# Kernel optimization log

Hardware: AMD Instinct MI355X
Metric: run time of the kernel (lower is better)

The kernel has to match this reference:

```python
import jax, jax.numpy as jnp
import numpy as np

N = 100_000   # nodes
E = 3_200_000 # edges
D = 128       # input feature dim


def setup_inputs() -> dict:
    key = jax.random.key(0)
    ks = jax.random.split(key, 6)
    x = jax.random.normal(ks[0], (N, D), dtype=jnp.float32)
    edge_index = jax.random.randint(ks[1], (2, E), 0, N, dtype=jnp.int32)
    # Glorot-ish init for the three GCN layer weights
    W1 = jax.random.normal(ks[2], (D, 32), dtype=jnp.float32) * (1.0 / np.sqrt(D))
    W2 = jax.random.normal(ks[3], (32, 16), dtype=jnp.float32) * (1.0 / np.sqrt(32))
    W3 = jax.random.normal(ks[4], (16, 1), dtype=jnp.float32) * (1.0 / np.sqrt(16))
    b1 = jnp.zeros((32,), jnp.float32)
    b2 = jnp.zeros((16,), jnp.float32)
    b3 = jnp.zeros((1,), jnp.float32)
    return {"x": x, "edge_index": edge_index, "W1": W1, "b1": b1,
            "W2": W2, "b2": b2, "W3": W3, "b3": b3}


def _gcn_edges(edge_index, num_nodes):
    # PyG GCNConv default: add self-loops, symmetric normalization
    loop = jnp.arange(num_nodes, dtype=edge_index.dtype)
    src = jnp.concatenate([edge_index[0], loop])
    dst = jnp.concatenate([edge_index[1], loop])
    deg = jax.ops.segment_sum(jnp.ones_like(dst, jnp.float32), dst, num_segments=num_nodes)
    dis = jax.lax.rsqrt(deg)  # deg >= 1 because of self-loops
    norm = dis[src] * dis[dst]  # [E+N]
    return src, dst, norm


def _gcn_layer(h, W, b, src, dst, norm, num_nodes):
    # linear transform, then normalized gather -> scatter-add aggregation
    hw = h @ W                                  # [N, out]
    msg = norm[:, None] * hw[src]               # [E+N, out]
    out = jax.ops.segment_sum(msg, dst, num_segments=num_nodes)
    return out + b


def reference(x, edge_index, W1, b1, W2, b2, W3, b3):
    src, dst, norm = _gcn_edges(edge_index, N)
    h = jax.nn.relu(_gcn_layer(x, W1, b1, src, dst, norm, N))
    h = jax.nn.relu(_gcn_layer(h, W2, b2, src, dst, norm, N))
    return _gcn_layer(h, W3, b3, src, dst, norm, N)  # [N, 1]
```

## Files before the change

kernel.cpp:

```cpp
#include <hip/hip_runtime.h>
#include <hip/hip_fp16.h>

#define NN 100000
#define NE 3200000
#define DI 128

#define RSH 8
#define RMASK 255
#define NB ((NN + RMASK) >> RSH)
#define CAP 9472
#define SB 256
#define SCHUNK ((NE + SB - 1) / SB)
#define MAXE ((SCHUNK + 1023) / 1024)
#define SK ((CAP + 1023) / 1024)

#define OFF_GCUR   ((size_t)100000)
#define OFF_ROWPTR ((size_t)100800)
#define OFF_DEG    ((size_t)200800)
#define OFF_REC    ((size_t)300800)
#define OFF_HWD1   (OFF_REC + (size_t)NB * CAP)
#define OFF_HWD2   (OFF_HWD1 + (size_t)16 * NN)
#define OFF_HWD3   (OFF_HWD2 + (size_t)8 * NN)

#define ACC8(r) { const __half2* hp_ = reinterpret_cast<const __half2*>(&(r));      \
    float2 f0_ = __half22float2(hp_[0]), f1_ = __half22float2(hp_[1]);              \
    float2 f2_ = __half22float2(hp_[2]), f3_ = __half22float2(hp_[3]);              \
    a0 += f0_.x; a1 += f0_.y; a2 += f1_.x; a3 += f1_.y;                             \
    a4 += f2_.x; a5 += f2_.y; a6 += f3_.x; a7 += f3_.y; }

__global__ __launch_bounds__(1024) void scatter_kernel(const int* __restrict__ src,
                                                       const int* __restrict__ dst,
                                                       int* __restrict__ gcur,
                                                       unsigned* __restrict__ rec) {
    __shared__ unsigned lrec[SCHUNK];
    __shared__ unsigned short lbkt[SCHUNK];
    __shared__ int lh[NB];
    __shared__ int lofs[NB];
    __shared__ int lbase[NB];
    int tid = threadIdx.x;
    for (int i = tid; i < NB; i += 1024) lh[i] = 0;
    __syncthreads();
    int base = blockIdx.x * SCHUNK;
    int end = min(base + SCHUNK, NE);
    int cnt_total = end - base;
    int keys[MAXE], rank[MAXE];
#pragma unroll
    for (int i = 0; i < MAXE; i++) {
        int e = base + tid + i * 1024;
        bool ok = e < end;
        keys[i] = ok ? dst[e] : 0;
        rank[i] = ok ? atomicAdd(&lh[keys[i] >> RSH], 1) : 0;
    }
    __syncthreads();
    int* stmp = (int*)lrec;
    int v = (tid < NB) ? lh[tid] : 0;
    stmp[tid] = v;
    __syncthreads();
    for (int d = 1; d < 1024; d <<= 1) {
        int t = (tid >= d) ? stmp[tid - d] : 0;
        __syncthreads();
        stmp[tid] += t;
        __syncthreads();
    }
    if (tid < NB) {
        lofs[tid] = stmp[tid] - v;
        lbase[tid] = v ? atomicAdd(&gcur[tid], v) : 0;
    }
    __syncthreads();
#pragma unroll
    for (int i = 0; i < MAXE; i++) {
        int e = base + tid + i * 1024;
        if (e < end) {
            int d = keys[i];
            int b = d >> RSH;
            int slot = lofs[b] + rank[i];
            lrec[slot] = ((unsigned)src[e] << RSH) | (unsigned)(d & RMASK);
            lbkt[slot] = (unsigned short)b;
        }
    }
    __syncthreads();
    for (int j = tid; j < cnt_total; j += 1024) {
        int b = lbkt[j];
        int pos = lbase[b] + (j - lofs[b]);
        if (pos < CAP)
            rec[(size_t)b * CAP + pos] = lrec[j];
    }
}

__global__ __launch_bounds__(1024) void sort_kernel(const int* __restrict__ gcur,
                                                    unsigned* __restrict__ rec,
                                                    int* __restrict__ rowptr,
                                                    int* __restrict__ deg,
                                                    float* __restrict__ dis) {
    __shared__ int cnt[256];
    __shared__ int sc[256];
    int tid = threadIdx.x, b = blockIdx.x;
    if (tid < 256) cnt[tid] = 0;
    __syncthreads();
    int count = min(gcur[b], CAP);
    size_t rbeg = (size_t)b * CAP;
    unsigned myrec[SK];
    int myrank[SK];
#pragma unroll
    for (int k = 0; k < SK; k++) {
        int j = tid + k * 1024;
        if (j < count) {
            unsigned r = rec[rbeg + j];
            myrec[k] = r;
            myrank[k] = atomicAdd(&cnt[r & RMASK], 1);
        } else {
            myrec[k] = 0; myrank[k] = 0;
        }
    }
    __syncthreads();
    if (tid < 256) sc[tid] = cnt[tid];
    __syncthreads();
    for (int d = 1; d < 256; d <<= 1) {
        int v = (tid < 256 && tid >= d) ? sc[tid - d] : 0;
        __syncthreads();
        if (tid < 256) sc[tid] += v;
        __syncthreads();
    }
    if (tid < 256) {
        int excl = sc[tid] - cnt[tid];
        int node = (b << RSH) + tid;
        if (node < NN) {
            rowptr[node] = (int)rbeg + excl;
            deg[node] = cnt[tid];
            dis[node] = rsqrtf((float)cnt[tid] + 1.0f);
        }
        cnt[tid] = excl;
    }
    __syncthreads();
#pragma unroll
    for (int k = 0; k < SK; k++) {
        int j = tid + k * 1024;
        if (j < count) {
            unsigned r = myrec[k];
            int pos = cnt[r & RMASK] + myrank[k];
            rec[rbeg + pos] = r >> RSH;
        }
    }
}

__global__ __launch_bounds__(256) void gemm1_kernel(const float* __restrict__ x,
                                                    const float* __restrict__ W,
                                                    const float* __restrict__ dis,
                                                    __half* __restrict__ out) {
    __shared__ float Ws[DI][32];
    __shared__ float xs[32][DI + 4];
    int tid = threadIdx.x;
    for (int i4 = tid; i4 < DI * 32 / 4; i4 += 256) {
        float4 w = reinterpret_cast<const float4*>(W)[i4];
        int base = i4 * 4;
        *reinterpret_cast<float4*>(&Ws[base / 32][base % 32]) = w;
    }
    int node0 = blockIdx.x * 32;
    for (int i4 = tid; i4 < 32 * DI / 4; i4 += 256) {
        int base = i4 * 4;
        int nl = base / DI, k = base % DI;
        int node = node0 + nl;
        float4 v = (node < NN) ? reinterpret_cast<const float4*>(x)[((size_t)node * DI + k) / 4]
                               : make_float4(0.f, 0.f, 0.f, 0.f);
        *reinterpret_cast<float4*>(&xs[nl][k]) = v;
    }
    __syncthreads();
    int nl = tid >> 3;
    int c4 = (tid & 7) * 4;
    int node = node0 + nl;
    if (node >= NN) return;
    float a0 = 0.f, a1 = 0.f, a2 = 0.f, a3 = 0.f;
#pragma unroll 8
    for (int k4 = 0; k4 < DI; k4 += 4) {
        float4 xv = *reinterpret_cast<const float4*>(&xs[nl][k4]);
        float4 w0 = *reinterpret_cast<const float4*>(&Ws[k4 + 0][c4]);
        float4 w1 = *reinterpret_cast<const float4*>(&Ws[k4 + 1][c4]);
        float4 w2 = *reinterpret_cast<const float4*>(&Ws[k4 + 2][c4]);
        float4 w3 = *reinterpret_cast<const float4*>(&Ws[k4 + 3][c4]);
        a0 += xv.x * w0.x + xv.y * w1.x + xv.z * w2.x + xv.w * w3.x;
        a1 += xv.x * w0.y + xv.y * w1.y + xv.z * w2.y + xv.w * w3.y;
        a2 += xv.x * w0.z + xv.y * w1.z + xv.z * w2.z + xv.w * w3.z;
        a3 += xv.x * w0.w + xv.y * w1.w + xv.z * w2.w + xv.w * w3.w;
    }
    float dn = dis[node];
    __half2 h0 = __floats2half2_rn(dn * a0, dn * a1);
    __half2 h1 = __floats2half2_rn(dn * a2, dn * a3);
    __half2* op = reinterpret_cast<__half2*>(out + (size_t)node * 32 + c4);
    op[0] = h0;
    op[1] = h1;
}

__global__ __launch_bounds__(256) void agg32_fused_kernel(const int* __restrict__ rowptr,
                                                          const int* __restrict__ deg,
                                                          const int* __restrict__ srcs,
                                                          const __half* __restrict__ hwd1,
                                                          const float* __restrict__ dis,
                                                          const float* __restrict__ b1,
                                                          const float* __restrict__ W2,
                                                          __half2* __restrict__ hwd2) {
    __shared__ float hc[64][33];
    __shared__ float W2s[32][16];
    int tid = threadIdx.x;
    for (int i = tid; i < 512; i += 256) W2s[i >> 4][i & 15] = W2[i];
    int gtid = blockIdx.x * 256 + tid;
    int node = gtid >> 2;
    int lane = tid & 3;
    int nl = tid >> 2;
    int c8 = lane * 8;
    if (node < NN) {
        int beg = rowptr[node];
        int end = beg + deg[node];
        const float4* hv = reinterpret_cast<const float4*>(hwd1);
        float a0, a1, a2, a3, a4, a5, a6, a7;
        {
            float4 sr = hv[(size_t)node * 4 + lane];
            const __half2* hp = reinterpret_cast<const __half2*>(&sr);
            float2 f0 = __half22float2(hp[0]), f1 = __half22float2(hp[1]);
            float2 f2 = __half22float2(hp[2]), f3 = __half22float2(hp[3]);
            a0 = f0.x; a1 = f0.y; a2 = f1.x; a3 = f1.y;
            a4 = f2.x; a5 = f2.y; a6 = f3.x; a7 = f3.y;
        }
        int j = beg;
        for (; j + 8 <= end; j += 8) {
            int i0 = srcs[j],     i1 = srcs[j + 1], i2 = srcs[j + 2], i3 = srcs[j + 3];
            int i4 = srcs[j + 4], i5 = srcs[j + 5], i6 = srcs[j + 6], i7 = srcs[j + 7];
            float4 r0 = hv[(size_t)i0 * 4 + lane];
            float4 r1 = hv[(size_t)i1 * 4 + lane];
            float4 r2 = hv[(size_t)i2 * 4 + lane];
            float4 r3 = hv[(size_t)i3 * 4 + lane];
            float4 r4 = hv[(size_t)i4 * 4 + lane];
            float4 r5 = hv[(size_t)i5 * 4 + lane];
            float4 r6 = hv[(size_t)i6 * 4 + lane];
            float4 r7 = hv[(size_t)i7 * 4 + lane];
            ACC8(r0); ACC8(r1); ACC8(r2); ACC8(r3);
            ACC8(r4); ACC8(r5); ACC8(r6); ACC8(r7);
        }
        for (; j < end; j++) {
            float4 r = hv[(size_t)srcs[j] * 4 + lane];
            ACC8(r);
        }
        float dn = dis[node];
        hc[nl][c8 + 0] = fmaxf(dn * a0 + b1[c8 + 0], 0.f);
        hc[nl][c8 + 1] = fmaxf(dn * a1 + b1[c8 + 1], 0.f);
        hc[nl][c8 + 2] = fmaxf(dn * a2 + b1[c8 + 2], 0.f);
        hc[nl][c8 + 3] = fmaxf(dn * a3 + b1[c8 + 3], 0.f);
        hc[nl][c8 + 4] = fmaxf(dn * a4 + b1[c8 + 4], 0.f);
        hc[nl][c8 + 5] = fmaxf(dn * a5 + b1[c8 + 5], 0.f);
        hc[nl][c8 + 6] = fmaxf(dn * a6 + b1[c8 + 6], 0.f);
        hc[nl][c8 + 7] = fmaxf(dn * a7 + b1[c8 + 7], 0.f);
    }
    __syncthreads();
    int node0 = blockIdx.x * 64;
    for (int o = tid; o < 64 * 8; o += 256) {
        int l = o >> 3, cp = o & 7;
        int n2 = node0 + l;
        if (n2 < NN) {
            float s0 = 0.f, s1 = 0.f;
#pragma unroll
            for (int k = 0; k < 32; k++) {
                float h = hc[l][k];
                s0 += h * W2s[k][2 * cp];
                s1 += h * W2s[k][2 * cp + 1];
            }
            float d2 = dis[n2];
            hwd2[(size_t)n2 * 8 + cp] = __floats2half2_rn(d2 * s0, d2 * s1);
        }
    }
}

__global__ __launch_bounds__(256) void agg16_fused_kernel(const int* __restrict__ rowptr,
                                                          const int* __restrict__ deg,
                                                          const int* __restrict__ srcs,
                                                          const __half* __restrict__ hwd2,
                                                          const float* __restrict__ dis,
                                                          const float* __restrict__ b2,
                                                          const float* __restrict__ W3,
                                                          __half* __restrict__ hwd3) {
    __shared__ float hc[128][17];
    __shared__ float W3s[16];
    int tid = threadIdx.x;
    if (tid < 16) W3s[tid] = W3[tid];
    int gtid = blockIdx.x * 256 + tid;
    int node = gtid >> 1;
    int lane = tid & 1;
    int nl = tid >> 1;
    int c8 = lane * 8;
    if (node < NN) {
        int beg = rowptr[node];
        int end = beg + deg[node];
        const float4* hv = reinterpret_cast<const float4*>(hwd2);
        float a0, a1, a2, a3, a4, a5, a6, a7;
        {
            float4 sr = hv[(size_t)node * 2 + lane];
            const __half2* hp = reinterpret_cast<const __half2*>(&sr);
            float2 f0 = __half22float2(hp[0]), f1 = __half22float2(hp[1]);
            float2 f2 = __half22float2(hp[2]), f3 = __half22float2(hp[3]);
            a0 = f0.x; a1 = f0.y; a2 = f1.x; a3 = f1.y;
            a4 = f2.x; a5 = f2.y; a6 = f3.x; a7 = f3.y;
        }
        int j = beg;
        for (; j + 8 <= end; j += 8) {
            int i0 = srcs[j],     i1 = srcs[j + 1], i2 = srcs[j + 2], i3 = srcs[j + 3];
            int i4 = srcs[j + 4], i5 = srcs[j + 5], i6 = srcs[j + 6], i7 = srcs[j + 7];
            float4 r0 = hv[(size_t)i0 * 2 + lane];
            float4 r1 = hv[(size_t)i1 * 2 + lane];
            float4 r2 = hv[(size_t)i2 * 2 + lane];
            float4 r3 = hv[(size_t)i3 * 2 + lane];
            float4 r4 = hv[(size_t)i4 * 2 + lane];
            float4 r5 = hv[(size_t)i5 * 2 + lane];
            float4 r6 = hv[(size_t)i6 * 2 + lane];
            float4 r7 = hv[(size_t)i7 * 2 + lane];
            ACC8(r0); ACC8(r1); ACC8(r2); ACC8(r3);
            ACC8(r4); ACC8(r5); ACC8(r6); ACC8(r7);
        }
        for (; j < end; j++) {
            float4 r = hv[(size_t)srcs[j] * 2 + lane];
            ACC8(r);
        }
        float dn = dis[node];
        hc[nl][c8 + 0] = fmaxf(dn * a0 + b2[c8 + 0], 0.f);
        hc[nl][c8 + 1] = fmaxf(dn * a1 + b2[c8 + 1], 0.f);
        hc[nl][c8 + 2] = fmaxf(dn * a2 + b2[c8 + 2], 0.f);
        hc[nl][c8 + 3] = fmaxf(dn * a3 + b2[c8 + 3], 0.f);
        hc[nl][c8 + 4] = fmaxf(dn * a4 + b2[c8 + 4], 0.f);
        hc[nl][c8 + 5] = fmaxf(dn * a5 + b2[c8 + 5], 0.f);
        hc[nl][c8 + 6] = fmaxf(dn * a6 + b2[c8 + 6], 0.f);
        hc[nl][c8 + 7] = fmaxf(dn * a7 + b2[c8 + 7], 0.f);
    }
    __syncthreads();
    int node0 = blockIdx.x * 128;
    if (tid < 128) {
        int n2 = node0 + tid;
        if (n2 < NN) {
            float s = 0.f;
#pragma unroll
            for (int k = 0; k < 16; k++) s += hc[tid][k] * W3s[k];
            hwd3[n2] = __float2half(dis[n2] * s);
        }
    }
}

__global__ __launch_bounds__(256) void agg1_kernel(const int* __restrict__ rowptr,
                                                   const int* __restrict__ deg,
                                                   const int* __restrict__ srcs,
                                                   const __half* __restrict__ hwd3,
                                                   const float* __restrict__ dis,
                                                   const float* __restrict__ b3,
                                                   float* __restrict__ out) {
    int node = blockIdx.x * 256 + threadIdx.x;
    if (node >= NN) return;
    int beg = rowptr[node];
    int end = beg + deg[node];
    float acc = __half2float(hwd3[node]);
    int j = beg;
    for (; j + 4 <= end; j += 4) {
        float v0 = __half2float(hwd3[srcs[j]]);
        float v1 = __half2float(hwd3[srcs[j + 1]]);
        float v2 = __half2float(hwd3[srcs[j + 2]]);
        float v3 = __half2float(hwd3[srcs[j + 3]]);
        acc += (v0 + v1) + (v2 + v3);
    }
    for (; j < end; j++) acc += __half2float(hwd3[srcs[j]]);
    out[node] = dis[node] * acc + b3[0];
}

extern "C" void kernel_launch(void* const* d_in, const int* in_sizes, int n_in,
                              void* d_out, int out_size, void* d_ws, size_t ws_size,
                              hipStream_t stream) {
    const float* x  = (const float*)d_in[0];
    const int*   ei = (const int*)d_in[1];
    const int*   src = ei;
    const int*   dst = ei + NE;
    const float* W1 = (const float*)d_in[2];
    const float* b1 = (const float*)d_in[3];
    const float* W2 = (const float*)d_in[4];
    const float* b2 = (const float*)d_in[5];
    const float* W3 = (const float*)d_in[6];
    const float* b3 = (const float*)d_in[7];
    float* out = (float*)d_out;
    float* ws  = (float*)d_ws;

    float*    dis    = ws;
    int*      gcur   = (int*)(ws + OFF_GCUR);
    int*      rowptr = (int*)(ws + OFF_ROWPTR);
    int*      deg    = (int*)(ws + OFF_DEG);
    unsigned* rec    = (unsigned*)(ws + OFF_REC);
    __half*   hwd1   = (__half*)(ws + OFF_HWD1);
    __half*   hwd2   = (__half*)(ws + OFF_HWD2);
    __half*   hwd3   = (__half*)(ws + OFF_HWD3);

    hipMemsetAsync(gcur, 0, NB * sizeof(int), stream);
    scatter_kernel<<<SB, 1024, 0, stream>>>(src, dst, gcur, rec);
    sort_kernel<<<NB, 1024, 0, stream>>>(gcur, rec, rowptr, deg, dis);
    gemm1_kernel<<<(NN + 31) / 32, 256, 0, stream>>>(x, W1, dis, hwd1);
    agg32_fused_kernel<<<((size_t)NN * 4 + 255) / 256, 256, 0, stream>>>(
        rowptr, deg, (const int*)rec, hwd1, dis, b1, W2, (__half2*)hwd2);
    agg16_fused_kernel<<<((size_t)NN * 2 + 255) / 256, 256, 0, stream>>>(
        rowptr, deg, (const int*)rec, hwd2, dis, b2, W3, hwd3);
    agg1_kernel<<<(NN + 255) / 256, 256, 0, stream>>>(rowptr, deg, (const int*)rec, hwd3, dis, b3, out);
}
```

Measured before the change: 172.4 us.

## Split layer-1 aggregation into two 16-feature planes with separate GEMM2

The 32-wide fp16 layer-1 feature table is stored as two 16-feature planes, and aggregation runs as two passes, one per plane. Each pass gathers a smaller table (3.2 MB instead of 6.4 MB), which is meant to improve cache hit rates for the random gathers. The fused W2 projection moves into a separate gemm2 kernel that reads the stored fp16 hidden activations. This adds two kernel launches, reads the edge lists twice, writes an extra intermediate, and rounds h1 to fp16 before the W2 projection.

```diff
diff --git a/kernel.cpp b/kernel.cpp
--- a/kernel.cpp
+++ b/kernel.cpp
@@ -18,8 +18,11 @@
 #define OFF_ROWPTR ((size_t)100800)
 #define OFF_DEG    ((size_t)200800)
 #define OFF_REC    ((size_t)300800)
-#define OFF_HWD1   (OFF_REC + (size_t)NB * CAP)
-#define OFF_HWD2   (OFF_HWD1 + (size_t)16 * NN)
+#define OFF_HWD1A  (OFF_REC + (size_t)NB * CAP)
+#define OFF_HWD1B  (OFF_HWD1A + (size_t)8 * NN)
+#define OFF_H1A    (OFF_HWD1B + (size_t)8 * NN)
+#define OFF_H1B    (OFF_H1A + (size_t)8 * NN)
+#define OFF_HWD2   (OFF_H1B + (size_t)8 * NN)
 #define OFF_HWD3   (OFF_HWD2 + (size_t)8 * NN)
 
 #define ACC8(r) { const __half2* hp_ = reinterpret_cast<const __half2*>(&(r));      \
@@ -146,7 +149,8 @@
 __global__ __launch_bounds__(256) void gemm1_kernel(const float* __restrict__ x,
                                                     const float* __restrict__ W,
                                                     const float* __restrict__ dis,
-                                                    __half* __restrict__ out) {
+                                                    __half2* __restrict__ hwd1a,
+                                                    __half2* __restrict__ hwd1b) {
     __shared__ float Ws[DI][32];
     __shared__ float xs[32][DI + 4];
     int tid = threadIdx.x;
@@ -185,87 +189,124 @@
     float dn = dis[node];
     __half2 h0 = __floats2half2_rn(dn * a0, dn * a1);
     __half2 h1 = __floats2half2_rn(dn * a2, dn * a3);
-    __half2* op = reinterpret_cast<__half2*>(out + (size_t)node * 32 + c4);
-    op[0] = h0;
-    op[1] = h1;
-}
-
-__global__ __launch_bounds__(256) void agg32_fused_kernel(const int* __restrict__ rowptr,
-                                                          const int* __restrict__ deg,
-                                                          const int* __restrict__ srcs,
-                                                          const __half* __restrict__ hwd1,
-                                                          const float* __restrict__ dis,
-                                                          const float* __restrict__ b1,
-                                                          const float* __restrict__ W2,
-                                                          __half2* __restrict__ hwd2) {
-    __shared__ float hc[64][33];
-    __shared__ float W2s[32][16];
+    __half2* dstp = (c4 < 16) ? hwd1a : hwd1b;
+    int cc = c4 & 15;
+    dstp[(size_t)node * 8 + (cc >> 1) + 0] = h0;
+    dstp[(size_t)node * 8 + (cc >> 1) + 1] = h1;
+}
+
+template <int FOFF>
+__global__ __launch_bounds__(256) void agg32_pass_kernel(const int* __restrict__ rowptr,
+                                                         const int* __restrict__ deg,
+                                                         const int* __restrict__ srcs,
+                                                         const __half* __restrict__ hwd1p,
+                                                         const float* __restrict__ dis,
+                                                         const float* __restrict__ b1,
+                                                         __half* __restrict__ h1p) {
+    int gtid = blockIdx.x * 256 + threadIdx.x;
+    int node = gtid >> 1;
+    int lane = gtid & 1;
+    if (node >= NN) return;
+    int c8 = lane * 8;
+    int beg = rowptr[node];
+    int end = beg + deg[node];
+    const float4* hv = reinterpret_cast<const float4*>(hwd1p);
+    float a0, a1, a2, a3, a4, a5, a6, a7;
+    {
+        float4 sr = hv[(size_t)node * 2 + lane];
+        const __half2* hp = reinterpret_cast<const __half2*>(&sr);
+        float2 f0 = __half22float2(hp[0]), f1 = __half22float2(hp[1]);
+        float2 f2 = __half22float2(hp[2]), f3 = __half22float2(hp[3]);
+        a0 = f0.x; a1 = f0.y; a2 = f1.x; a3 = f1.y;
+        a4 = f2.x; a5 = f2.y; a6 = f3.x; a7 = f3.y;
+    }
+    int j = beg;
+    for (; j + 8 <= end; j += 8) {
+        int i0 = srcs[j],     i1 = srcs[j + 1], i2 = srcs[j + 2], i3 = srcs[j + 3];
+        int i4 = srcs[j + 4], i5 = srcs[j + 5], i6 = srcs[j + 6], i7 = srcs[j + 7];
+        float4 r0 = hv[(size_t)i0 * 2 + lane];
+        float4 r1 = hv[(size_t)i1 * 2 + lane];
+        float4 r2 = hv[(size_t)i2 * 2 + lane];
+        float4 r3 = hv[(size_t)i3 * 2 + lane];
+        float4 r4 = hv[(size_t)i4 * 2 + lane];
+        float4 r5 = hv[(size_t)i5 * 2 + lane];
+        float4 r6 = hv[(size_t)i6 * 2 + lane];
+        float4 r7 = hv[(size_t)i7 * 2 + lane];
+        ACC8(r0); ACC8(r1); ACC8(r2); ACC8(r3);
+        ACC8(r4); ACC8(r5); ACC8(r6); ACC8(r7);
+    }
+    for (; j < end; j++) {
+        float4 r = hv[(size_t)srcs[j] * 2 + lane];
+        ACC8(r);
+    }
+    float dn = dis[node];
+    float r0 = fmaxf(dn * a0 + b1[FOFF + c8 + 0], 0.f);
+    float r1 = fmaxf(dn * a1 + b1[FOFF + c8 + 1], 0.f);
+    float r2 = fmaxf(dn * a2 + b1[FOFF + c8 + 2], 0.f);
+    float r3 = fmaxf(dn * a3 + b1[FOFF + c8 + 3], 0.f);
+    float r4 = fmaxf(dn * a4 + b1[FOFF + c8 + 4], 0.f);
+    float r5 = fmaxf(dn * a5 + b1[FOFF + c8 + 5], 0.f);
+    float r6 = fmaxf(dn * a6 + b1[FOFF + c8 + 6], 0.f);
+    float r7 = fmaxf(dn * a7 + b1[FOFF + c8 + 7], 0.f);
+    float4 outv;
+    __half2* op = reinterpret_cast<__half2*>(&outv);
+    op[0] = __floats2half2_rn(r0, r1);
+    op[1] = __floats2half2_rn(r2, r3);
+    op[2] = __floats2half2_rn(r4, r5);
+    op[3] = __floats2half2_rn(r6, r7);
+    reinterpret_cast<float4*>(h1p)[(size_t)node * 2 + lane] = outv;
+}
+
+__global__ __launch_bounds__(256) void gemm2_kernel(const __half* __restrict__ h1a,
+                                                    const __half* __restrict__ h1b,
+                                                    const float* __restrict__ W2,
+                                                    const float* __restrict__ dis,
+                                                    __half2* __restrict__ hwd2) {
+    __shared__ float Ws[32][16];
+    __shared__ float xs[64][36];
     int tid = threadIdx.x;
-    for (int i = tid; i < 512; i += 256) W2s[i >> 4][i & 15] = W2[i];
-    int gtid = blockIdx.x * 256 + tid;
-    int node = gtid >> 2;
-    int lane = tid & 3;
-    int nl = tid >> 2;
-    int c8 = lane * 8;
-    if (node < NN) {
-        int beg = rowptr[node];
-        int end = beg + deg[node];
-        const float4* hv = reinterpret_cast<const float4*>(hwd1);
-        float a0, a1, a2, a3, a4, a5, a6, a7;
-        {
-            float4 sr = hv[(size_t)node * 4 + lane];
-            const __half2* hp = reinterpret_cast<const __half2*>(&sr);
-            float2 f0 = __half22float2(hp[0]), f1 = __half22float2(hp[1]);
-            float2 f2 = __half22float2(hp[2]), f3 = __half22float2(hp[3]);
-            a0 = f0.x; a1 = f0.y; a2 = f1.x; a3 = f1.y;
-            a4 = f2.x; a5 = f2.y; a6 = f3.x; a7 = f3.y;
-        }
-        int j = beg;
-        for (; j + 8 <= end; j += 8) {
-            int i0 = srcs[j],     i1 = srcs[j + 1], i2 = srcs[j + 2], i3 = srcs[j + 3];
-            int i4 = srcs[j + 4], i5 = srcs[j + 5], i6 = srcs[j + 6], i7 = srcs[j + 7];
-            float4 r0 = hv[(size_t)i0 * 4 + lane];
-            float4 r1 = hv[(size_t)i1 * 4 + lane];
-            float4 r2 = hv[(size_t)i2 * 4 + lane];
-            float4 r3 = hv[(size_t)i3 * 4 + lane];
-            float4 r4 = hv[(size_t)i4 * 4 + lane];
-            float4 r5 = hv[(size_t)i5 * 4 + lane];
-            float4 r6 = hv[(size_t)i6 * 4 + lane];
-            float4 r7 = hv[(size_t)i7 * 4 + lane];
-            ACC8(r0); ACC8(r1); ACC8(r2); ACC8(r3);
-            ACC8(r4); ACC8(r5); ACC8(r6); ACC8(r7);
-        }
-        for (; j < end; j++) {
-            float4 r = hv[(size_t)srcs[j] * 4 + lane];
-            ACC8(r);
-        }
-        float dn = dis[node];
-        hc[nl][c8 + 0] = fmaxf(dn * a0 + b1[c8 + 0], 0.f);
-        hc[nl][c8 + 1] = fmaxf(dn * a1 + b1[c8 + 1], 0.f);
-        hc[nl][c8 + 2] = fmaxf(dn * a2 + b1[c8 + 2], 0.f);
-        hc[nl][c8 + 3] = fmaxf(dn * a3 + b1[c8 + 3], 0.f);
-        hc[nl][c8 + 4] = fmaxf(dn * a4 + b1[c8 + 4], 0.f);
-        hc[nl][c8 + 5] = fmaxf(dn * a5 + b1[c8 + 5], 0.f);
-        hc[nl][c8 + 6] = fmaxf(dn * a6 + b1[c8 + 6], 0.f);
-        hc[nl][c8 + 7] = fmaxf(dn * a7 + b1[c8 + 7], 0.f);
-    }
-    __syncthreads();
+    if (tid < 128) {
+        float4 w = reinterpret_cast<const float4*>(W2)[tid];
+        int base = tid * 4;
+        *reinterpret_cast<float4*>(&Ws[base / 16][base % 16]) = w;
+    }
     int node0 = blockIdx.x * 64;
-    for (int o = tid; o < 64 * 8; o += 256) {
-        int l = o >> 3, cp = o & 7;
-        int n2 = node0 + l;
-        if (n2 < NN) {
-            float s0 = 0.f, s1 = 0.f;
-#pragma unroll
-            for (int k = 0; k < 32; k++) {
-                float h = hc[l][k];
-                s0 += h * W2s[k][2 * cp];
-                s1 += h * W2s[k][2 * cp + 1];
-            }
-            float d2 = dis[n2];
-            hwd2[(size_t)n2 * 8 + cp] = __floats2half2_rn(d2 * s0, d2 * s1);
-        }
-    }
+    {
+        int nl = tid >> 2, q = tid & 3;
+        int plane = q >> 1, half = q & 1;
+        int node = node0 + nl;
+        const __half* srcp = plane ? h1b : h1a;
+        float4 v = (node < NN) ? reinterpret_cast<const float4*>(srcp)[(size_t)node * 2 + half]
+                               : make_float4(0.f, 0.f, 0.f, 0.f);
+        const __half2* hp = reinterpret_cast<const __half2*>(&v);
+        float2 f0 = __half22float2(hp[0]), f1 = __half22float2(hp[1]);
+        float2 f2 = __half22float2(hp[2]), f3 = __half22float2(hp[3]);
+        int cb = plane * 16 + half * 8;
+        float4 s0 = make_float4(f0.x, f0.y, f1.x, f1.y);
+        float4 s1 = make_float4(f2.x, f2.y, f3.x, f3.y);
+        *reinterpret_cast<float4*>(&xs[nl][cb + 0]) = s0;
+        *reinterpret_cast<float4*>(&xs[nl][cb + 4]) = s1;
+    }
+    __syncthreads();
+    int nl = tid >> 2, c4 = (tid & 3) * 4;
+    int node = node0 + nl;
+    if (node >= NN) return;
+    float a0 = 0.f, a1 = 0.f, a2 = 0.f, a3 = 0.f;
+#pragma unroll
+    for (int k4 = 0; k4 < 32; k4 += 4) {
+        float4 xv = *reinterpret_cast<const float4*>(&xs[nl][k4]);
+        float4 w0 = *reinterpret_cast<const float4*>(&Ws[k4 + 0][c4]);
+        float4 w1 = *reinterpret_cast<const float4*>(&Ws[k4 + 1][c4]);
+        float4 w2 = *reinterpret_cast<const float4*>(&Ws[k4 + 2][c4]);
+        float4 w3 = *reinterpret_cast<const float4*>(&Ws[k4 + 3][c4]);
+        a0 += xv.x * w0.x + xv.y * w1.x + xv.z * w2.x + xv.w * w3.x;
+        a1 += xv.x * w0.y + xv.y * w1.y + xv.z * w2.y + xv.w * w3.y;
+        a2 += xv.x * w0.z + xv.y * w1.z + xv.z * w2.z + xv.w * w3.z;
+        a3 += xv.x * w0.w + xv.y * w1.w + xv.z * w2.w + xv.w * w3.w;
+    }
+    float dn = dis[node];
+    hwd2[(size_t)node * 8 + (c4 >> 1) + 0] = __floats2half2_rn(dn * a0, dn * a1);
+    hwd2[(size_t)node * 8 + (c4 >> 1) + 1] = __floats2half2_rn(dn * a2, dn * a3);
 }
 
 __global__ __launch_bounds__(256) void agg16_fused_kernel(const int* __restrict__ rowptr,
@@ -385,16 +426,22 @@
     int*      rowptr = (int*)(ws + OFF_ROWPTR);
     int*      deg    = (int*)(ws + OFF_DEG);
     unsigned* rec    = (unsigned*)(ws + OFF_REC);
-    __half*   hwd1   = (__half*)(ws + OFF_HWD1);
+    __half*   hwd1a  = (__half*)(ws + OFF_HWD1A);
+    __half*   hwd1b  = (__half*)(ws + OFF_HWD1B);
+    __half*   h1a    = (__half*)(ws + OFF_H1A);
+    __half*   h1b    = (__half*)(ws + OFF_H1B);
     __half*   hwd2   = (__half*)(ws + OFF_HWD2);
     __half*   hwd3   = (__half*)(ws + OFF_HWD3);
 
     hipMemsetAsync(gcur, 0, NB * sizeof(int), stream);
     scatter_kernel<<<SB, 1024, 0, stream>>>(src, dst, gcur, rec);
     sort_kernel<<<NB, 1024, 0, stream>>>(gcur, rec, rowptr, deg, dis);
-    gemm1_kernel<<<(NN + 31) / 32, 256, 0, stream>>>(x, W1, dis, hwd1);
-    agg32_fused_kernel<<<((size_t)NN * 4 + 255) / 256, 256, 0, stream>>>(
-        rowptr, deg, (const int*)rec, hwd1, dis, b1, W2, (__half2*)hwd2);
+    gemm1_kernel<<<(NN + 31) / 32, 256, 0, stream>>>(x, W1, dis, (__half2*)hwd1a, (__half2*)hwd1b);
+    agg32_pass_kernel<0><<<((size_t)NN * 2 + 255) / 256, 256, 0, stream>>>(
+        rowptr, deg, (const int*)rec, hwd1a, dis, b1, h1a);
+    agg32_pass_kernel<16><<<((size_t)NN * 2 + 255) / 256, 256, 0, stream>>>(
+        rowptr, deg, (const int*)rec, hwd1b, dis, b1, h1b);
+    gemm2_kernel<<<(NN + 63) / 64, 256, 0, stream>>>(h1a, h1b, W2, dis, (__half2*)hwd2);
     agg16_fused_kernel<<<((size_t)NN * 2 + 255) / 256, 256, 0, stream>>>(
         rowptr, deg, (const int*)rec, hwd2, dis, b2, W3, hwd3);
     agg1_kernel<<<(NN + 255) / 256, 256, 0, stream>>>(rowptr, deg, (const int*)rec, hwd3, dis, b3, out);
```

Measured after the change: 196.2 us. 13.8% more time.
